# Kernel optimization log

Measured on AMD Instinct MI355X. Metric: run time of the kernel, lower is better.

The kernel has to match this reference:

```python
import jax, jax.numpy as jnp
import numpy as np

RHO_MAX = 28
Z_MAX = 14
N = RHO_MAX                 # rho grid points (rho = 1..N)
M = 2 * Z_MAX + 1           # z grid points
K = N * M                   # flattened grid size
BATCH = 8


def _build_operators():
    """Vectorized construction of the banded finite-difference operators
    (equivalent to the module's double python loop)."""
    rho = np.arange(1, N + 1, dtype=np.float32)      # RHO values, independent of j
    I = np.eye(K, dtype=np.float32)
    # d^2/drho^2: neighbors at i+-1 (flat offset +-M), all j valid
    dd_rho = -2.0 * I + np.eye(K, k=M, dtype=np.float32) + np.eye(K, k=-M, dtype=np.float32)
    # d^2/dz^2: neighbors at j+-1 (flat offset +-1), but not across rho-row boundaries
    off = np.zeros(K - 1, dtype=np.float32)
    off[np.arange(K - 1) % M != M - 1] = 1.0
    dd_z = -2.0 * I + np.diag(off, 1) + np.diag(off, -1)
    # (1/rho) d/drho: forward difference, diag -1/rho_i, superdiag(+M) +1/rho_i (i<N-1)
    inv_rho_flat = np.repeat(1.0 / rho, M)           # [K]
    inv_rho_d_rho = np.diag(-inv_rho_flat) + np.diag(inv_rho_flat[: K - M], M)
    laplacian = -(dd_rho + inv_rho_d_rho + dd_z)
    return laplacian.astype(np.float32), inv_rho_flat.astype(np.float32)


def setup_inputs() -> dict:
    key = jax.random.key(0)
    k1, k2 = jax.random.split(key)
    laplacian_np, inv_rho_np = _build_operators()
    return {
        "num_nucleons": jax.random.randint(k1, (BATCH, 1), 0, 50, dtype=jnp.int32),
        "mean_fields": jax.random.normal(k2, (BATCH, N, M), dtype=jnp.float32),
        "laplacian": jnp.asarray(laplacian_np),
        "inv_rho": jnp.asarray(inv_rho_np),
        "max_alpha": 4,
    }


def reference(num_nucleons, mean_fields, laplacian, inv_rho, max_alpha):
    B, n, m = mean_fields.shape
    Kk = n * m
    v = mean_fields.reshape(B, Kk)                                   # diagonal potential
    alphas = jnp.arange(max_alpha + 1, dtype=mean_fields.dtype)      # [A]
    # V_eff[a,b,k] = v[b,k] + (alpha * 1/rho_k)^2  (zero extra term for alpha=0)
    V_eff = v[None, :, :] + (alphas[:, None, None] * inv_rho[None, None, :]) ** 2.0
    idx = jnp.arange(Kk)
    A = jnp.broadcast_to(laplacian, (max_alpha + 1, B, Kk, Kk))
    A = A.at[..., idx, idx].add(V_eff)                               # H = -lap_op + V_eff on diag
    w = jnp.real(jnp.linalg.eigvals(A))                              # [A,B,K]
    # torch concat is alpha-major then hstack regroups per batch -> [B, A*K]
    eig = jnp.transpose(w, (1, 0, 2)).reshape(B, (max_alpha + 1) * Kk)
    eig = jnp.sort(eig, axis=1)
    # mask: only column 0 filled with clip(num_nucleons[:,0], 0, 2)
    occ = jnp.clip(num_nucleons[:, 0], 0, 2).astype(eig.dtype)
    binding = (eig[:, 0] * occ)[:, None]                             # [B,1]
    return binding
```

## Files before the change

### kernel.cpp

```cpp
#include <hip/hip_runtime.h>
#include <math.h>

#define NRHO 28
#define NZ   29
#define KK   (NRHO * NZ)
#define BATCH 8
#define MLAN  24
#define NL    15


template <int CTRL>
__device__ __forceinline__ float dpp_mov(float x) {
    int y = __builtin_amdgcn_update_dpp(
        0, __builtin_bit_cast(int, x), CTRL, 0xF, 0xF, true);
    return __builtin_bit_cast(float, y);
}
template <int CTRL>
__device__ __forceinline__ float dpp_add(float x) { return x + dpp_mov<CTRL>(x); }

__device__ __forceinline__ float wave_sum(float x) {
    x = dpp_add<0x111>(x);
    x = dpp_add<0x112>(x);
    x = dpp_add<0x114>(x);
    x = dpp_add<0x118>(x);
    x = dpp_add<0x142>(x);
    x = dpp_add<0x143>(x);
    int ti = __builtin_amdgcn_readlane(__builtin_bit_cast(int, x), 63);
    return __builtin_bit_cast(float, ti);
}

__device__ __forceinline__ void wave_sum2(float& x, float& y) {
    x = dpp_add<0x111>(x);  y = dpp_add<0x111>(y);
    x = dpp_add<0x112>(x);  y = dpp_add<0x112>(y);
    x = dpp_add<0x114>(x);  y = dpp_add<0x114>(y);
    x = dpp_add<0x118>(x);  y = dpp_add<0x118>(y);
    x = dpp_add<0x142>(x);  y = dpp_add<0x142>(y);
    x = dpp_add<0x143>(x);  y = dpp_add<0x143>(y);
    int xi = __builtin_amdgcn_readlane(__builtin_bit_cast(int, x), 63);
    int yi = __builtin_amdgcn_readlane(__builtin_bit_cast(int, y), 63);
    x = __builtin_bit_cast(float, xi);
    y = __builtin_bit_cast(float, yi);
}

__device__ __forceinline__ void lanczos_step(
    int it, float (&cur)[NL], float (&prev)[NL], const float (&cd)[NL],
    float cru, float cz, float czP13, float czB, bool hsel, int psel,
    float& rcpn_prev, float& ginv_prev,
    float* al_s, float* bsq_s, int t)
{
    float vsend = hsel ? cur[0] : cur[NL - 1];
    float vrecv = __shfl(vsend, psel, 64);

    float w[NL];
#pragma unroll
    for (int j = 0; j < NL; ++j) {
        float t1 = cru * cur[j];
        float dn = dpp_mov<0x138>(t1);
        float vS = dpp_mov<0x130>(cur[j]);
        w[j] = cd[j] * cur[j] + dn + cru * vS;
    }
#pragma unroll
    for (int j = 0; j < NL - 2; ++j) {
        w[j]     += cz * cur[j + 1];
        w[j + 1] += cz * cur[j];
    }
    w[NL - 2] += czP13 * cur[NL - 1];
    w[NL - 1] += czP13 * cur[NL - 2];
    if (hsel) w[0]      += czB * vrecv;
    else      w[NL - 1] += czB * vrecv;

    float x0 = 0.f, x1 = 0.f, y0 = 0.f, y1 = 0.f;
#pragma unroll
    for (int j = 0; j < NL; ++j) {
        if (j & 1) { x1 += w[j] * cur[j]; y1 += cur[j] * cur[j]; }
        else       { x0 += w[j] * cur[j]; y0 += cur[j] * cur[j]; }
    }
    float x = x0 + x1, y = y0 + y1;
    wave_sum2(x, y);

    float rcpy = __builtin_amdgcn_rcpf(y);
    float a = x * rcpy;
    float b = (it == 0) ? 0.f : y * rcpn_prev * ginv_prev;
    if (t == 0) {
        al_s[it] = a;
        if (it > 0) bsq_s[it - 1] = b * ginv_prev;
    }

    int e = ((__builtin_bit_cast(int, y) >> 23) & 0xFF) - 127;
    int eh = e >> 1;
    float g    = __builtin_bit_cast(float, (127 - eh) << 23);
    float ginv = __builtin_bit_cast(float, (127 + eh) << 23);

    float ga = g * a, gb = g * b;
#pragma unroll
    for (int j = 0; j < NL; ++j)
        prev[j] = g * w[j] - ga * cur[j] - gb * prev[j];

    rcpn_prev = rcpy; ginv_prev = ginv;
}

__global__ __launch_bounds__(64, 1) void lanczos_min_eig(
    const int*   __restrict__ nn,
    const float* __restrict__ mf,
    const float* __restrict__ lap,
    float*       __restrict__ out)
{
    const int b = blockIdx.x;
    const int t = threadIdx.x;
    const int h = t / 28;
    const int r = t % 28;
    const bool alive = (t < 56);
    const int z0 = (h == 1) ? 15 : 0;

    __shared__ float al_s[MLAN];
    __shared__ float bsq_s[MLAN];

    float cd[NL], va[NL], vb[NL];
    float cru = 0.f, cz = 0.f, czP13 = 0.f, czB = 0.f;
    int psel = t;
    bool hsel = (h == 1);
#pragma unroll
    for (int j = 0; j < NL; ++j) { cd[j] = 0.f; va[j] = vb[j] = 0.f; }

    float s0 = 0.f;
    if (alive) {
        const int p0 = r * NZ + z0;
        const float lapd = lap[(size_t)p0 * KK + p0];
        cz = lap[(size_t)p0 * KK + p0 + 1];
        if (r < NRHO - 1) {
            float u = lap[(size_t)p0 * KK + p0 + NZ];
            float l = lap[(size_t)(p0 + NZ) * KK + p0];
            float s = sqrtf(fmaxf(u * l, 0.f));
            cru = (u < 0.f) ? -s : s;
        }
        {
            int p14 = r * NZ + 14;
            czB = lap[(size_t)p14 * KK + p14 + 1];
        }
        czP13 = (h == 0) ? cz : 0.f;
        psel = (h == 0) ? (t + 28) : (t - 28);

        const int nv = (h == 1) ? 14 : 15;
        for (int j = 0; j < nv; ++j) {
            int p = p0 + j;
            cd[j] = lapd + mf[b * KK + p];
            va[j] = 1.0f;
            s0 += 1.0f;
        }
    }

    {
        float s = wave_sum(s0);
        float inv = rsqrtf(s);
#pragma unroll
        for (int j = 0; j < NL; ++j) va[j] *= inv;
    }

    float rcpn_prev = 1.f, ginv_prev = 1.f;
#pragma unroll 1
    for (int it = 0; it < MLAN; it += 2) {
        lanczos_step(it,     va, vb, cd, cru, cz, czP13, czB, hsel, psel,
                     rcpn_prev, ginv_prev, al_s, bsq_s, t);
        lanczos_step(it + 1, vb, va, cd, cru, cz, czP13, czB, hsel, psel,
                     rcpn_prev, ginv_prev, al_s, bsq_s, t);
    }
    __syncthreads();

    float glo = 1e30f, ghi = -1e30f;
    for (int i = t; i < MLAN; i += 64) {
        float a_ = al_s[i];
        float bl = (i > 0)        ? sqrtf(bsq_s[i - 1]) : 0.f;
        float br = (i < MLAN - 1) ? sqrtf(bsq_s[i])     : 0.f;
        glo = fminf(glo, a_ - bl - br);
        ghi = fmaxf(ghi, a_ + bl + br);
    }
#pragma unroll
    for (int m = 1; m < 64; m <<= 1) {
        glo = fminf(glo, __shfl_xor(glo, m, 64));
        ghi = fmaxf(ghi, __shfl_xor(ghi, m, 64));
    }

    float lo = glo, hi = ghi;
    for (int rd = 0; rd < 3; ++rd) {
        float wdt = (hi - lo) * 0.015625f;
        float x = lo + wdt * (float)(t + 1);
        float d = al_s[0] - x;
        int cnt = (d < 0.f) ? 1 : 0;
        for (int i = 1; i < MLAN; ++i) {
            float ad = fabsf(d);
            if (ad < 1e-20f) d = (d < 0.f) ? -1e-20f : 1e-20f;
            d = (al_s[i] - x) - bsq_s[i - 1] * __builtin_amdgcn_rcpf(d);
            cnt += (d < 0.f) ? 1 : 0;
        }
        float cx = (cnt >= 1) ? x : 1e30f;
#pragma unroll
        for (int m = 1; m < 64; m <<= 1) cx = fminf(cx, __shfl_xor(cx, m, 64));
        if (cx < 1e29f) {
            hi = cx;
            lo = cx - wdt;
        } else {
            lo = lo + wdt * 64.0f;
        }
    }

    if (t == 0) {
        int o = nn[b];
        o = (o < 0) ? 0 : ((o > 2) ? 2 : o);
        out[b] = 0.5f * (lo + hi) * (float)o;
    }
}

extern "C" void kernel_launch(void* const* d_in, const int* in_sizes, int n_in,
                              void* d_out, int out_size, void* d_ws, size_t ws_size,
                              hipStream_t stream) {
    const int*   nn  = (const int*)d_in[0];
    const float* mf  = (const float*)d_in[1];
    const float* lap = (const float*)d_in[2];
    float* out = (float*)d_out;

    hipLaunchKernelGGL(lanczos_min_eig, dim3(BATCH), dim3(64), 0, stream,
                       nn, mf, lap, out);
}
```

Before: 75.75 us.

## Carry A*v alongside Lanczos vector to overlap reductions with matvec

Restructures the Lanczos recurrence to keep both v and A*v. Each step computes the dot products first from the stored A*v, then computes A*(A*v) while the wave reduction is pending, and updates both recurrences. The intent is to take the matvec off the critical path before the cross-lane reduction so the two latencies overlap. In exchange it needs twice the vector registers and an extra axpy per step, and propagating A*v by recurrence can cost some numerical accuracy.

```diff
diff --git a/kernel.cpp b/kernel.cpp
--- a/kernel.cpp
+++ b/kernel.cpp
@@ -43,48 +43,47 @@
 }
 
 __device__ __forceinline__ void lanczos_step(
-    int it, float (&cur)[NL], float (&prev)[NL], const float (&cd)[NL],
+    int it, float (&cur)[NL], float (&prev)[NL],
+    float (&acur)[NL], float (&aprev)[NL],
+    const float (&cd)[NL],
     float cru, float cz, float czP13, float czB, bool hsel, int psel,
     float& rcpn_prev, float& ginv_prev,
     float* al_s, float* bsq_s, int t)
 {
-    float vsend = hsel ? cur[0] : cur[NL - 1];
+    float vsend = hsel ? acur[0] : acur[NL - 1];
     float vrecv = __shfl(vsend, psel, 64);
 
-    float w[NL];
+    float x0 = 0.f, x1 = 0.f, y0 = 0.f, y1 = 0.f;
 #pragma unroll
     for (int j = 0; j < NL; ++j) {
-        float t1 = cru * cur[j];
+        if (j & 1) { x1 += acur[j] * cur[j]; y1 += cur[j] * cur[j]; }
+        else       { x0 += acur[j] * cur[j]; y0 += cur[j] * cur[j]; }
+    }
+    float x = x0 + x1, y = y0 + y1;
+
+    float z[NL];
+#pragma unroll
+    for (int j = 0; j < NL; ++j) {
+        float t1 = cru * acur[j];
         float dn = dpp_mov<0x138>(t1);
-        float vS = dpp_mov<0x130>(cur[j]);
-        w[j] = cd[j] * cur[j] + dn + cru * vS;
+        float vS = dpp_mov<0x130>(acur[j]);
+        z[j] = cd[j] * acur[j] + dn + cru * vS;
     }
 #pragma unroll
     for (int j = 0; j < NL - 2; ++j) {
-        w[j]     += cz * cur[j + 1];
-        w[j + 1] += cz * cur[j];
-    }
-    w[NL - 2] += czP13 * cur[NL - 1];
-    w[NL - 1] += czP13 * cur[NL - 2];
-    if (hsel) w[0]      += czB * vrecv;
-    else      w[NL - 1] += czB * vrecv;
-
-    float x0 = 0.f, x1 = 0.f, y0 = 0.f, y1 = 0.f;
-#pragma unroll
-    for (int j = 0; j < NL; ++j) {
-        if (j & 1) { x1 += w[j] * cur[j]; y1 += cur[j] * cur[j]; }
-        else       { x0 += w[j] * cur[j]; y0 += cur[j] * cur[j]; }
-    }
-    float x = x0 + x1, y = y0 + y1;
+        z[j]     += cz * acur[j + 1];
+        z[j + 1] += cz * acur[j];
+    }
+    z[NL - 2] += czP13 * acur[NL - 1];
+    z[NL - 1] += czP13 * acur[NL - 2];
+    if (hsel) z[0]      += czB * vrecv;
+    else      z[NL - 1] += czB * vrecv;
+
     wave_sum2(x, y);
 
     float rcpy = __builtin_amdgcn_rcpf(y);
     float a = x * rcpy;
     float b = (it == 0) ? 0.f : y * rcpn_prev * ginv_prev;
-    if (t == 0) {
-        al_s[it] = a;
-        if (it > 0) bsq_s[it - 1] = b * ginv_prev;
-    }
 
     int e = ((__builtin_bit_cast(int, y) >> 23) & 0xFF) - 127;
     int eh = e >> 1;
@@ -93,8 +92,15 @@
 
     float ga = g * a, gb = g * b;
 #pragma unroll
-    for (int j = 0; j < NL; ++j)
-        prev[j] = g * w[j] - ga * cur[j] - gb * prev[j];
+    for (int j = 0; j < NL; ++j) {
+        prev[j]  = g * acur[j] - ga * cur[j]  - gb * prev[j];
+        aprev[j] = g * z[j]    - ga * acur[j] - gb * aprev[j];
+    }
+
+    if (t == 0) {
+        al_s[it] = a;
+        if (it > 0) bsq_s[it - 1] = b * ginv_prev;
+    }
 
     rcpn_prev = rcpy; ginv_prev = ginv;
 }
@@ -115,12 +121,12 @@
     __shared__ float al_s[MLAN];
     __shared__ float bsq_s[MLAN];
 
-    float cd[NL], va[NL], vb[NL];
+    float cd[NL], va[NL], vb[NL], wa[NL], wb[NL];
     float cru = 0.f, cz = 0.f, czP13 = 0.f, czB = 0.f;
     int psel = t;
     bool hsel = (h == 1);
 #pragma unroll
-    for (int j = 0; j < NL; ++j) { cd[j] = 0.f; va[j] = vb[j] = 0.f; }
+    for (int j = 0; j < NL; ++j) { cd[j] = 0.f; va[j] = vb[j] = wa[j] = wb[j] = 0.f; }
 
     float s0 = 0.f;
     if (alive) {
@@ -156,13 +162,34 @@
         for (int j = 0; j < NL; ++j) va[j] *= inv;
     }
 
+    {
+        float vsend = hsel ? va[0] : va[NL - 1];
+        float vrecv = __shfl(vsend, psel, 64);
+#pragma unroll
+        for (int j = 0; j < NL; ++j) {
+            float t1 = cru * va[j];
+            float dn = dpp_mov<0x138>(t1);
+            float vS = dpp_mov<0x130>(va[j]);
+            wa[j] = cd[j] * va[j] + dn + cru * vS;
+        }
+#pragma unroll
+        for (int j = 0; j < NL - 2; ++j) {
+            wa[j]     += cz * va[j + 1];
+            wa[j + 1] += cz * va[j];
+        }
+        wa[NL - 2] += czP13 * va[NL - 1];
+        wa[NL - 1] += czP13 * va[NL - 2];
+        if (hsel) wa[0]      += czB * vrecv;
+        else      wa[NL - 1] += czB * vrecv;
+    }
+
     float rcpn_prev = 1.f, ginv_prev = 1.f;
 #pragma unroll 1
     for (int it = 0; it < MLAN; it += 2) {
-        lanczos_step(it,     va, vb, cd, cru, cz, czP13, czB, hsel, psel,
-                     rcpn_prev, ginv_prev, al_s, bsq_s, t);
-        lanczos_step(it + 1, vb, va, cd, cru, cz, czP13, czB, hsel, psel,
-                     rcpn_prev, ginv_prev, al_s, bsq_s, t);
+        lanczos_step(it,     va, vb, wa, wb, cd, cru, cz, czP13, czB, hsel,
+                     psel, rcpn_prev, ginv_prev, al_s, bsq_s, t);
+        lanczos_step(it + 1, vb, va, wb, wa, cd, cru, cz, czP13, czB, hsel,
+                     psel, rcpn_prev, ginv_prev, al_s, bsq_s, t);
     }
     __syncthreads();
 
```

Result: no change. 77.20 us (+1.9%).
